# Kernel tuning notes

Measured on AMD Instinct MI355X. Metric: run time of the kernel, lower is better.

The kernel has to match this reference:

```python
import jax, jax.numpy as jnp
import numpy as np
import math

INPUT_SIZE = 20
HIDDEN = 1500
OUTPUT = 20
MLP_HID = math.ceil(5 / 4 * HIDDEN)  # 1875
T = 4096


def setup_inputs() -> dict:
    key = jax.random.key(0)
    ks = jax.random.split(key, 10)
    s_lstm = 1.0 / np.sqrt(HIDDEN)
    s1 = 1.0 / np.sqrt(HIDDEN)
    s2 = 1.0 / np.sqrt(MLP_HID)
    return {
        "input_seq": jax.random.normal(ks[0], (T, INPUT_SIZE), dtype=jnp.float32),
        "W_ih": jax.random.uniform(ks[1], (4 * HIDDEN, INPUT_SIZE), jnp.float32, -s_lstm, s_lstm),
        "W_hh": jax.random.uniform(ks[2], (4 * HIDDEN, HIDDEN), jnp.float32, -s_lstm, s_lstm),
        "b_ih": jax.random.uniform(ks[3], (4 * HIDDEN,), jnp.float32, -s_lstm, s_lstm),
        "b_hh": jax.random.uniform(ks[4], (4 * HIDDEN,), jnp.float32, -s_lstm, s_lstm),
        "W1": jax.random.uniform(ks[5], (MLP_HID, HIDDEN), jnp.float32, -s1, s1),
        "b1": jax.random.uniform(ks[6], (MLP_HID,), jnp.float32, -s1, s1),
        "W2": jax.random.uniform(ks[7], (OUTPUT, MLP_HID), jnp.float32, -s2, s2),
        "b2": jax.random.uniform(ks[8], (OUTPUT,), jnp.float32, -s2, s2),
    }


def reference(input_seq, W_ih, W_hh, b_ih, b_hh, W1, b1, W2, b2):
    H = W_hh.shape[1]
    # Precompute input contribution for all timesteps: (T, 4H)
    x_proj = input_seq @ W_ih.T + (b_ih + b_hh)

    def step(carry, xp):
        h, c = carry
        gates = xp + h @ W_hh.T  # (4H,)
        i, f, g, o = jnp.split(gates, 4)
        i = jax.nn.sigmoid(i)
        f = jax.nn.sigmoid(f)
        g = jnp.tanh(g)
        o = jax.nn.sigmoid(o)
        c_new = f * c + i * g
        h_new = o * jnp.tanh(c_new)
        return (h_new, c_new), None

    h0 = jnp.zeros((H,), dtype=input_seq.dtype)
    c0 = jnp.zeros((H,), dtype=input_seq.dtype)
    (h_last, _), _ = jax.lax.scan(step, (h0, c0), x_proj)
    # Dropout is identity in eval mode. Module returns predictions[-1],
    # which only depends on the last hidden state.
    hid = h_last @ W1.T + b1
    return hid @ W2.T + b2
```

## Files before the change

### kernel.cpp

```cpp
#include <hip/hip_runtime.h>
#include <math.h>

#define TT 4096
#define HH 1500
#define NB 250
#define NT 512
#define NREP 8

typedef unsigned uv4 __attribute__((ext_vector_type(4)));
typedef _Float16 h2f __attribute__((ext_vector_type(2)));

#define ALD4(p)   __hip_atomic_load((p), __ATOMIC_RELAXED, __HIP_MEMORY_SCOPE_AGENT)
#define AST4(p,v) __hip_atomic_store((p), (v), __ATOMIC_RELAXED, __HIP_MEMORY_SCOPE_AGENT)

__device__ __forceinline__ float fast_sigmoid(float z) {
  return 1.0f / (1.0f + __expf(-z));
}
__device__ __forceinline__ float fast_tanh(float z) {
  float az = fabsf(z);
  float e  = __expf(-2.0f * az);
  float r  = (1.0f - e) / (1.0f + e);
  return copysignf(r, z);
}
__device__ __forceinline__ float dot2(unsigned wb, unsigned hb, float acc) {
#if __has_builtin(__builtin_amdgcn_fdot2)
  return __builtin_amdgcn_fdot2(__builtin_bit_cast(h2f, wb),
                                __builtin_bit_cast(h2f, hb), acc, false);
#else
  h2f w = __builtin_bit_cast(h2f, wb), h = __builtin_bit_cast(h2f, hb);
  acc = fmaf((float)w.x, (float)h.x, acc);
  return fmaf((float)w.y, (float)h.y, acc);
#endif
}

__global__
__attribute__((amdgpu_flat_work_group_size(NT, NT), amdgpu_waves_per_eu(2, 2)))
void lstm_fused(
    const float* __restrict__ x,
    const float* __restrict__ Wih,
    const float* __restrict__ Whh,
    const float* __restrict__ bih,
    const float* __restrict__ bhh,
    const float* __restrict__ W1,
    const float* __restrict__ b1,
    const float* __restrict__ W2,
    const float* __restrict__ b2,
    float* __restrict__ out,
    unsigned* __restrict__ ws)
{
  const int tid = threadIdx.x;
  const int bid = blockIdx.x;
  const int wv  = tid >> 6;
  const int ln  = tid & 63;

  unsigned* pub  = ws;
  unsigned* hidp = ws + NREP * 2 * 1536;

  __shared__ __align__(16) _Float16 lds_wh[24 * 1536];
  __shared__ __align__(16) _Float16 lds_hh[1536];
  __shared__ __align__(16) float    lds_hf[1536];
  __shared__ float lds_xp[2][24];
  __shared__ float lds_gs[4][6];
  float* lds_hd = (float*)lds_wh;

  for (int hi = tid; hi < 24 * 1536; hi += NT) {
    const int r = hi / 1536, k = hi - r * 1536;
    const int u = r >> 2, g = r & 3;
    const size_t grow = (size_t)(g * HH + bid * 6 + u) * HH;
    const float v = (k < HH) ? Whh[grow + k] : 0.f;
    lds_wh[hi] = (_Float16)v;
  }

  const int uu = (wv < 6) ? wv : 0;
  const uv4* wp = ((const uv4*)lds_wh) + (size_t)uu * 4 * 192;
  const uv4* hp = (const uv4*)lds_hh;

  float4 wx0, wx1, wx2, wx3, wx4;
  float4 xr0, xr1, xr2, xr3, xr4;
  float bias = 0.f;
  if (wv == 6 && ln < 24) {
    const int g = ln / 6, u = ln - g * 6;
    const int row = g * HH + bid * 6 + u;
    const float4* s = (const float4*)(Wih + row * 20);
    wx0 = s[0]; wx1 = s[1]; wx2 = s[2]; wx3 = s[3]; wx4 = s[4];
    bias = bih[row] + bhh[row];
    const float4* xx = (const float4*)x;
    xr0 = xx[0]; xr1 = xx[1]; xr2 = xx[2]; xr3 = xx[3]; xr4 = xx[4];
  }

  float c = 0.f;

  if (tid < 6 * NREP)
    AST4(pub + (tid / 6) * 3072 + 6 * bid + (tid % 6), 1u);

  __syncthreads();

  unsigned* myrep = pub + (bid & (NREP - 1)) * 3072;

  for (int t = 0; t < TT; ++t) {
    const int s = t & 1;
    const unsigned tag = (unsigned)((t + 1) & 15);

    uv4 pw[12];
    if (wv < 6) {
      #pragma unroll
      for (int g = 0; g < 4; ++g) {
        #pragma unroll
        for (int m = 0; m < 3; ++m) pw[g * 3 + m] = wp[g * 192 + ln + 64 * m];
      }
    } else {
      if (wv == 6 && ln < 24) {
        float sx = bias;
        sx += wx0.x*xr0.x + wx0.y*xr0.y + wx0.z*xr0.z + wx0.w*xr0.w;
        sx += wx1.x*xr1.x + wx1.y*xr1.y + wx1.z*xr1.z + wx1.w*xr1.w;
        sx += wx2.x*xr2.x + wx2.y*xr2.y + wx2.z*xr2.z + wx2.w*xr2.w;
        sx += wx3.x*xr3.x + wx3.y*xr3.y + wx3.z*xr3.z + wx3.w*xr3.w;
        sx += wx4.x*xr4.x + wx4.y*xr4.y + wx4.z*xr4.z + wx4.w*xr4.w;
        lds_xp[s][ln] = sx;
      }
      const int p = tid - 384;
      unsigned* base = myrep + s * 1536;
      unsigned vals[12];
      for (;;) {
        unsigned miss = 0u;
        #pragma unroll
        for (int k = 0; k < 12; ++k) {
          const int idx = p + 128 * k;
          vals[k] = ALD4(base + idx);
          if (idx < HH) miss |= (vals[k] & 15u) ^ tag;
        }
        if (!__any(miss != 0u)) break;
        __builtin_amdgcn_s_sleep(1);
      }
      #pragma unroll
      for (int k = 0; k < 12; ++k) {
        const int idx = p + 128 * k;
        lds_hh[idx] = (idx < HH) ? (_Float16)__uint_as_float(vals[k])
                                 : (_Float16)0.f;
      }
    }
    __syncthreads();

    if (wv < 6) {
      uv4 hv[3];
      #pragma unroll
      for (int m = 0; m < 3; ++m) hv[m] = hp[ln + 64 * m];
      float a[4] = {0.f, 0.f, 0.f, 0.f};
      #pragma unroll
      for (int g = 0; g < 4; ++g) {
        #pragma unroll
        for (int m = 0; m < 3; ++m) {
          const uv4 q = pw[g * 3 + m], h = hv[m];
          a[g] = dot2(q.x, h.x, a[g]);
          a[g] = dot2(q.y, h.y, a[g]);
          a[g] = dot2(q.z, h.z, a[g]);
          a[g] = dot2(q.w, h.w, a[g]);
        }
      }
      #pragma unroll
      for (int g = 0; g < 4; ++g) {
        a[g] += __shfl_xor(a[g], 16, 64);
        a[g] += __shfl_xor(a[g], 32, 64);
      }
      const int q4 = ln >> 4;
      float v = (q4 == 0) ? a[0] : (q4 == 1) ? a[1] : (q4 == 2) ? a[2] : a[3];
      v += __shfl_xor(v, 1, 64);
      v += __shfl_xor(v, 2, 64);
      v += __shfl_xor(v, 4, 64);
      v += __shfl_xor(v, 8, 64);
      if ((ln & 15) == 0) lds_gs[q4][wv] = v;
    } else if (wv == 6 && ln < 24 && (t + 1) < TT) {
      const float4* xx = (const float4*)(x + 20 * (t + 1));
      xr0 = xx[0]; xr1 = xx[1]; xr2 = xx[2]; xr3 = xx[3]; xr4 = xx[4];
    }
    __syncthreads();

    if (wv == 7) {
      unsigned bits = 0u;
      if (ln < 6) {
        const int u = ln;
        const float zi = lds_gs[0][u] + lds_xp[s][0 + u];
        const float zf = lds_gs[1][u] + lds_xp[s][6 + u];
        const float zg = lds_gs[2][u] + lds_xp[s][12 + u];
        const float zo = lds_gs[3][u] + lds_xp[s][18 + u];
        const float ig = fast_sigmoid(zi);
        const float fg = fast_sigmoid(zf);
        const float gg = fast_tanh(zg);
        const float og = fast_sigmoid(zo);
        c = fg * c + ig * gg;
        const float hn = og * fast_tanh(c);
        bits = (__float_as_uint(hn) & ~15u) | (unsigned)((t + 2) & 15);
      }
      const int u6 = ln % 6;
      const unsigned myb = (unsigned)__shfl((int)bits, u6, 64);
      if (ln < 6 * NREP) {
        const int rep = ln / 6;
        AST4(pub + rep * 3072 + ((t + 1) & 1) * 1536 + 6 * bid + u6, myb);
      }
    }
  }

  if (wv >= 6) {
    const unsigned tagf = (unsigned)((TT + 1) & 15);
    const int p = tid - 384;
    unsigned* base = myrep;
    unsigned vals[12];
    for (;;) {
      unsigned miss = 0u;
      #pragma unroll
      for (int k = 0; k < 12; ++k) {
        const int idx = p + 128 * k;
        vals[k] = ALD4(base + idx);
        if (idx < HH) miss |= (vals[k] & 15u) ^ tagf;
      }
      if (!__any(miss != 0u)) break;
      __builtin_amdgcn_s_sleep(1);
    }
    #pragma unroll
    for (int k = 0; k < 12; ++k) {
      const int idx = p + 128 * k;
      lds_hf[idx] = (idx < HH) ? __uint_as_float(vals[k]) : 0.f;
    }
  }
  __syncthreads();

  {
    const float4* h4 = (const float4*)lds_hf;
    const int r = bid + 250 * wv;
    if (r < 1875) {
      const float4* wrow = (const float4*)(W1 + (size_t)r * HH);
      float ss = 0.f;
      #pragma unroll
      for (int m = 0; m < 6; ++m) {
        const int idx = ln + 64 * m;
        if (idx < 375) {
          const float4 a = wrow[idx], hv = h4[idx];
          ss += a.x*hv.x + a.y*hv.y + a.z*hv.z + a.w*hv.w;
        }
      }
      #pragma unroll
      for (int off = 32; off > 0; off >>= 1) ss += __shfl_xor(ss, off, 64);
      if (ln == 0) {
        const float vv = ss + b1[r];
        AST4(hidp + r, (__float_as_uint(vv) & ~15u) | 5u);
      }
    }
  }
  if (bid != 0) return;

  __syncthreads();
  for (int j = tid; j < 1875; j += NT) {
    unsigned bts;
    for (;;) {
      bts = ALD4(hidp + j);
      if ((bts & 15u) == 5u) break;
      __builtin_amdgcn_s_sleep(1);
    }
    lds_hd[j] = __uint_as_float(bts);
  }
  __syncthreads();

  for (int r = wv; r < 20; r += 8) {
    float ss = 0.f;
    for (int k = ln; k < 1875; k += 64)
      ss = fmaf(W2[(size_t)r * 1875 + k], lds_hd[k], ss);
    #pragma unroll
    for (int off = 32; off > 0; off >>= 1) ss += __shfl_xor(ss, off, 64);
    if (ln == 0) out[r] = ss + b2[r];
  }
}

extern "C" void kernel_launch(void* const* d_in, const int* in_sizes, int n_in,
                              void* d_out, int out_size, void* d_ws, size_t ws_size,
                              hipStream_t stream) {
  const float* x   = (const float*)d_in[0];
  const float* Wih = (const float*)d_in[1];
  const float* Whh = (const float*)d_in[2];
  const float* bih = (const float*)d_in[3];
  const float* bhh = (const float*)d_in[4];
  const float* W1  = (const float*)d_in[5];
  const float* b1  = (const float*)d_in[6];
  const float* W2  = (const float*)d_in[7];
  const float* b2  = (const float*)d_in[8];
  float* out   = (float*)d_out;
  unsigned* ws = (unsigned*)d_ws;

  hipLaunchKernelGGL(lstm_fused, dim3(NB), dim3(NT), 0, stream,
                     x, Wih, Whh, bih, bhh, W1, b1, W2, b2, out, ws);
}
```

Baseline: 11.21 ms.

## Spread hidden-state polling across compute waves with vectorized cache-bypassing loads

Moves the per-step polling for the published hidden-state vector off the two dedicated waves and onto the six compute waves. Each lane now spins on its own 16-byte chunk using an inline-asm global_load_dwordx4 with sc0 sc1 cache bits, instead of 12 scalar atomic loads per thread combined with a wave-wide any-vote. The aim is to cut polling latency and serial load count on the critical recurrence path. The risk is that compute waves now stall on polling, the inline asm relies on sc-bit semantics for coherence, and padding zeros are written once at start rather than every step.

```diff
diff --git a/kernel.cpp b/kernel.cpp
--- a/kernel.cpp
+++ b/kernel.cpp
@@ -9,6 +9,7 @@
 
 typedef unsigned uv4 __attribute__((ext_vector_type(4)));
 typedef _Float16 h2f __attribute__((ext_vector_type(2)));
+typedef _Float16 h4f __attribute__((ext_vector_type(4)));
 
 #define ALD4(p)   __hip_atomic_load((p), __ATOMIC_RELAXED, __HIP_MEMORY_SCOPE_AGENT)
 #define AST4(p,v) __hip_atomic_store((p), (v), __ATOMIC_RELAXED, __HIP_MEMORY_SCOPE_AGENT)
@@ -31,6 +32,22 @@
   acc = fmaf((float)w.x, (float)h.x, acc);
   return fmaf((float)w.y, (float)h.y, acc);
 #endif
+}
+
+__device__ __forceinline__ uv4 pollld(const unsigned* a) {
+  uv4 v;
+  asm volatile("global_load_dwordx4 %0, %1, off sc0 sc1\n\t"
+               "s_waitcnt vmcnt(0)"
+               : "=&v"(v) : "v"(a) : "memory");
+  return v;
+}
+__device__ __forceinline__ h4f cvt4h(uv4 v) {
+  h4f r;
+  r.x = (_Float16)__uint_as_float(v.x);
+  r.y = (_Float16)__uint_as_float(v.y);
+  r.z = (_Float16)__uint_as_float(v.z);
+  r.w = (_Float16)__uint_as_float(v.w);
+  return r;
 }
 
 __global__
@@ -70,6 +87,7 @@
     const float v = (k < HH) ? Whh[grow + k] : 0.f;
     lds_wh[hi] = (_Float16)v;
   }
+  if (tid < 36) lds_hh[1500 + tid] = (_Float16)0.f;
 
   const int uu = (wv < 6) ? wv : 0;
   const uv4* wp = ((const uv4*)lds_wh) + (size_t)uu * 4 * 192;
@@ -108,36 +126,27 @@
         #pragma unroll
         for (int m = 0; m < 3; ++m) pw[g * 3 + m] = wp[g * 192 + ln + 64 * m];
       }
-    } else {
-      if (wv == 6 && ln < 24) {
-        float sx = bias;
-        sx += wx0.x*xr0.x + wx0.y*xr0.y + wx0.z*xr0.z + wx0.w*xr0.w;
-        sx += wx1.x*xr1.x + wx1.y*xr1.y + wx1.z*xr1.z + wx1.w*xr1.w;
-        sx += wx2.x*xr2.x + wx2.y*xr2.y + wx2.z*xr2.z + wx2.w*xr2.w;
-        sx += wx3.x*xr3.x + wx3.y*xr3.y + wx3.z*xr3.z + wx3.w*xr3.w;
-        sx += wx4.x*xr4.x + wx4.y*xr4.y + wx4.z*xr4.z + wx4.w*xr4.w;
-        lds_xp[s][ln] = sx;
-      }
-      const int p = tid - 384;
-      unsigned* base = myrep + s * 1536;
-      unsigned vals[12];
-      for (;;) {
-        unsigned miss = 0u;
-        #pragma unroll
-        for (int k = 0; k < 12; ++k) {
-          const int idx = p + 128 * k;
-          vals[k] = ALD4(base + idx);
-          if (idx < HH) miss |= (vals[k] & 15u) ^ tag;
+      const int ck = (wv << 6) | ln;
+      if (ck < 375) {
+        unsigned* ap = myrep + s * 1536 + (ck << 2);
+        uv4 v;
+        for (;;) {
+          v = pollld(ap);
+          const unsigned miss = ((v.x & 15u) ^ tag) | ((v.y & 15u) ^ tag)
+                              | ((v.z & 15u) ^ tag) | ((v.w & 15u) ^ tag);
+          if (!miss) break;
+          __builtin_amdgcn_s_sleep(1);
         }
-        if (!__any(miss != 0u)) break;
-        __builtin_amdgcn_s_sleep(1);
-      }
-      #pragma unroll
-      for (int k = 0; k < 12; ++k) {
-        const int idx = p + 128 * k;
-        lds_hh[idx] = (idx < HH) ? (_Float16)__uint_as_float(vals[k])
-                                 : (_Float16)0.f;
-      }
+        *(h4f*)(lds_hh + (ck << 2)) = cvt4h(v);
+      }
+    } else if (wv == 6 && ln < 24) {
+      float sx = bias;
+      sx += wx0.x*xr0.x + wx0.y*xr0.y + wx0.z*xr0.z + wx0.w*xr0.w;
+      sx += wx1.x*xr1.x + wx1.y*xr1.y + wx1.z*xr1.z + wx1.w*xr1.w;
+      sx += wx2.x*xr2.x + wx2.y*xr2.y + wx2.z*xr2.z + wx2.w*xr2.w;
+      sx += wx3.x*xr3.x + wx3.y*xr3.y + wx3.z*xr3.z + wx3.w*xr3.w;
+      sx += wx4.x*xr4.x + wx4.y*xr4.y + wx4.z*xr4.z + wx4.w*xr4.w;
+      lds_xp[s][ln] = sx;
     }
     __syncthreads();
 
@@ -200,26 +209,24 @@
     }
   }
 
-  if (wv >= 6) {
+  {
     const unsigned tagf = (unsigned)((TT + 1) & 15);
-    const int p = tid - 384;
-    unsigned* base = myrep;
-    unsigned vals[12];
-    for (;;) {
-      unsigned miss = 0u;
-      #pragma unroll
-      for (int k = 0; k < 12; ++k) {
-        const int idx = p + 128 * k;
-        vals[k] = ALD4(base + idx);
-        if (idx < HH) miss |= (vals[k] & 15u) ^ tagf;
-      }
-      if (!__any(miss != 0u)) break;
-      __builtin_amdgcn_s_sleep(1);
-    }
-    #pragma unroll
-    for (int k = 0; k < 12; ++k) {
-      const int idx = p + 128 * k;
-      lds_hf[idx] = (idx < HH) ? __uint_as_float(vals[k]) : 0.f;
+    if (tid < 375) {
+      unsigned* ap = myrep + (tid << 2);
+      uv4 v;
+      for (;;) {
+        v = pollld(ap);
+        const unsigned miss = ((v.x & 15u) ^ tagf) | ((v.y & 15u) ^ tagf)
+                            | ((v.z & 15u) ^ tagf) | ((v.w & 15u) ^ tagf);
+        if (!miss) break;
+        __builtin_amdgcn_s_sleep(1);
+      }
+      float4 f = {__uint_as_float(v.x), __uint_as_float(v.y),
+                  __uint_as_float(v.z), __uint_as_float(v.w)};
+      *(float4*)(lds_hf + (tid << 2)) = f;
+    } else if (tid < 384) {
+      float4 z4 = {0.f, 0.f, 0.f, 0.f};
+      *(float4*)(lds_hf + (tid << 2)) = z4;
     }
   }
   __syncthreads();
```

Result: faster. 10.75 ms (-4.1%).
